# Kernel tuning notes

Hardware: AMD Instinct MI355X
Metric: run time of the kernel (lower is better)

The kernel has to match this reference:

```python
import jax, jax.numpy as jnp
import numpy as np

# Model dims
T, B, J, H, K, N_LAYERS = 512, 64, 256, 256, 25, 3
THETA = 1.0        # spike threshold
SIGMA_INIT = 0.5   # Dcls gaussian sigma (frozen, requires_grad=False)
EPS = 1e-5         # batchnorm eps
ALPHA = 5.0        # ATan surrogate alpha


@jax.custom_vjp
def atan_spike(v):
    # Heaviside forward, ATan surrogate backward (spikingjelly ATan, alpha=5)
    return (v > 0.0).astype(v.dtype)

def _atan_fwd(v):
    return atan_spike(v), v

def _atan_bwd(v, g):
    return (g * (ALPHA / 2.0) / (1.0 + (jnp.pi / 2.0 * ALPHA * v) ** 2),)

atan_spike.defvjp(_atan_fwd, _atan_bwd)


def gauss_kernel(W, P, sig):
    # Dcls1d version='gauss', kernel_count=1: gaussian-interpolated dense kernel.
    # W, P: (O, Jin) -> kernel (O, Jin, K)
    pos = jnp.arange(K, dtype=W.dtype)                  # dilated kernel positions
    c = P + K // 2                                      # shift P into [0, K)
    s = jnp.abs(sig) + 0.27                             # DCLS sigma floor
    g = jnp.exp(-0.5 * ((pos[None, None, :] - c[..., None]) / s) ** 2)
    g = g / (jnp.sum(g, axis=-1, keepdims=True) + 1e-7)  # normalize over positions
    return W[..., None] * g


def delay_lif_layer(x, W, P, beta, gamma, bb, U0):
    # x: (T, B, Jin) -> (T, B, O)
    kern = gauss_kernel(W, P, SIGMA_INIT)               # (O, Jin, K)
    xc = jnp.transpose(x, (1, 2, 0))                    # (B, Jin, T)
    y = jax.lax.conv_general_dilated(
        xc, kern, window_strides=(1,), padding=[(K - 1, 0)],  # causal left-pad
        dimension_numbers=('NCH', 'OIH', 'NCH'))        # (B, O, T)
    y = jnp.transpose(y, (2, 0, 1))                     # (T, B, O)
    # BatchNorm1d over the flattened (T*B) dim, per channel (training stats)
    mu = jnp.mean(y, axis=(0, 1))
    var = jnp.var(y, axis=(0, 1))
    y = (y - mu) * jax.lax.rsqrt(var + EPS) * gamma + bb

    # Soft-reset LIF recurrence over time (note: original passes RAW beta,
    # not sigmoid(beta), to the cell -- reproduced faithfully here).
    def step(carry, xt):
        Ut, St = carry
        Ut = beta * (Ut - THETA * St) + (1.0 - beta) * xt
        St = atan_spike(Ut - THETA)
        return (Ut, St), St

    _, o = jax.lax.scan(step, (U0, jnp.zeros_like(U0)), y)
    return o


def setup_inputs():
    key = jax.random.key(0)
    ks = jax.random.split(key, 5)
    # sparse binary spike input, [T, B, J]
    x = (jax.random.uniform(ks[0], (T, B, J)) < 0.2).astype(jnp.float32)
    bound = float(np.sqrt(6.0 / J))  # kaiming_uniform, relu gain, fan_in = J*1
    W = jax.random.uniform(ks[1], (N_LAYERS, H, J), minval=-bound, maxval=bound, dtype=jnp.float32)
    P = jax.random.uniform(ks[2], (N_LAYERS, H, J), minval=-(K // 2), maxval=K // 2, dtype=jnp.float32)
    beta = jax.random.uniform(ks[3], (N_LAYERS, H), minval=0.7, maxval=0.9, dtype=jnp.float32)
    gamma = jnp.ones((N_LAYERS, H), jnp.float32)
    bb = jnp.zeros((N_LAYERS, H), jnp.float32)
    U0 = jax.random.uniform(ks[4], (N_LAYERS, B, H), dtype=jnp.float32)  # RandomBatchwiseInit(0,1)
    return {"x": x, "W": W, "P": P, "beta": beta, "gamma": gamma, "bb": bb, "U0": U0}


def reference(x, W, P, beta, gamma, bb, U0):
    o = x
    for l in range(N_LAYERS):  # fixed small layer loop
        o = delay_lif_layer(o, W[l], P[l], beta[l], gamma[l], bb[l], U0[l])
    return o
```

## Files before the change

### kernel.cpp

```cpp
#include <hip/hip_runtime.h>
#include <math.h>

#define T_DIM 512
#define B_DIM 64
#define J_DIM 256
#define H_DIM 256
#define K_TAP 25
#define NL    3
#define M_DIM (T_DIM*B_DIM)
#define NBH   (B_DIM*H_DIM)
#define STATB 128
#define GUARD_ROWS 1536
#define GUARD_BYTES (GUARD_ROWS*J_DIM)

#define MB 128
#define NB 64
#define BK 64
#define NST (K_TAP*(J_DIM/BK))
#define BUFB 20480

typedef __attribute__((ext_vector_type(4))) int   i32x4;

__device__ __forceinline__ void gl16(const void* g, void* l){
  __builtin_amdgcn_global_load_lds((const __attribute__((address_space(1))) unsigned int*)g,
                                   (__attribute__((address_space(3))) unsigned int*)l, 16, 0, 0);
}

__global__ void zero_guard_k(unsigned char* __restrict__ g){
  *(uint4*)(g + (size_t)(blockIdx.x*256 + threadIdx.x)*16) = (uint4){0,0,0,0};
}

__global__ void cast_u8_k(const float* __restrict__ x, unsigned char* __restrict__ s){
  const int i = blockIdx.x*256 + threadIdx.x;
  const float4 v = *(const float4*)(x + (size_t)i*4);
  uchar4 o; o.x=(unsigned char)v.x; o.y=(unsigned char)v.y;
  o.z=(unsigned char)v.z; o.w=(unsigned char)v.w;
  *(uchar4*)(s + (size_t)i*4) = o;
}

__global__ void build_kern_k(const float* __restrict__ W, const float* __restrict__ P,
                             signed char* __restrict__ k0, signed char* __restrict__ k1,
                             signed char* __restrict__ k2, float* __restrict__ fsc, int layer){
  __shared__ float red[256];
  const int o = blockIdx.x, j = threadIdx.x;
  const float w = W[(layer*H_DIM + o)*J_DIM + j];
  const float p = P[(layer*H_DIM + o)*J_DIM + j];
  const float c = p + 12.0f;
  const float sg = 0.77f;
  float v[K_TAP]; float ssum = 0.f;
#pragma unroll
  for(int k=0;k<K_TAP;k++){ float z = ((float)k - c)/sg; v[k] = expf(-0.5f*z*z); ssum += v[k]; }
  const float inv = 1.0f/(ssum + 1e-7f);
  float mv = 0.f;
#pragma unroll
  for(int k=0;k<K_TAP;k++){ v[k] = w * (v[k]*inv); mv = fmaxf(mv, fabsf(v[k])); }
  red[j] = mv; __syncthreads();
  for(int st=128; st; st>>=1){ if(j<st) red[j] = fmaxf(red[j], red[j+st]); __syncthreads(); }
  int e; frexpf(red[0], &e);
  const float invq = ldexpf(1.f, 22 - e);
#pragma unroll
  for(int k=0;k<K_TAP;k++){
    const int d = (K_TAP-1)-k;
    int q = (int)lrintf(v[k]*invq);
    const int b0 = (int)(signed char)(q & 0xFF); q = (q - b0) >> 8;
    const int b1 = (int)(signed char)(q & 0xFF); q = (q - b1) >> 8;
    const size_t idx = (size_t)(d*H_DIM + o)*J_DIM + j;
    k0[idx] = (signed char)b0; k1[idx] = (signed char)b1; k2[idx] = (signed char)q;
  }
  if(j==0) fsc[o] = ldexpf(1.f, e - 22);
}

__global__ __launch_bounds__(256,2) void conv_mfma_k(const unsigned char* __restrict__ spk,
    const signed char* __restrict__ k0, const signed char* __restrict__ k1,
    const signed char* __restrict__ k2, const float* __restrict__ fsc,
    float* __restrict__ y){
  __shared__ unsigned char lds[3][BUFB];
  const int tid = threadIdx.x, lane = tid & 63, wave = tid >> 6;
  const int bid = blockIdx.x;
  const int q   = (bid & 7)*128 + (bid >> 3);
  const int m0  = (q & 255) * MB;
  const int n0  = (q >> 8) * NB;
  const int wm0 = (wave >> 1) << 6;
  const int wn0 = (wave & 1) << 5;

  const int srow  = tid >> 2;
  const int sslot = ((tid & 3) ^ (srow >> 1)) & 3;
  const int rslot = ((((lane>>4) ^ (lane>>1)) & 3) << 4);

  i32x4 acc0[4][2], acc1[4][2], acc2[4][2];
#pragma unroll
  for(int m=0;m<4;m++)
#pragma unroll
    for(int n=0;n<2;n++){
      acc0[m][n] = (i32x4){0,0,0,0};
      acc1[m][n] = (i32x4){0,0,0,0};
      acc2[m][n] = (i32x4){0,0,0,0};
    }

#define STAGE(base,t) do{ \
    const int d_ = (t)>>2, jc_ = ((t)&3)<<6; \
    unsigned char* lb_ = (base); \
    const unsigned char* as_ = spk + (size_t)(m0 + srow - (d_<<6) + GUARD_ROWS)*J_DIM + jc_ + sslot*16; \
    gl16(as_,                    lb_        + wave*1024); \
    gl16(as_ + (size_t)64*J_DIM, lb_ + 4096 + wave*1024); \
    const size_t bo_ = (size_t)(d_*H_DIM + n0 + srow)*J_DIM + jc_ + sslot*16; \
    gl16(k0 + bo_, lb_ + 8192  + wave*1024); \
    gl16(k1 + bo_, lb_ + 12288 + wave*1024); \
    gl16(k2 + bo_, lb_ + 16384 + wave*1024); \
  }while(0)

  unsigned char* const L = &lds[0][0];

  STAGE(L, 0);
  STAGE(L + BUFB, 1);

  int rb = 0;
  for(int t=0; t<NST; ++t){
    if(t < NST-1) asm volatile("s_waitcnt vmcnt(5)" ::: "memory");
    else          asm volatile("s_waitcnt vmcnt(0)" ::: "memory");
    __builtin_amdgcn_s_barrier();
    __builtin_amdgcn_sched_barrier(0);
    unsigned char* Lb = L + rb*BUFB;
    i32x4 af[4], b0f[2], b1f[2], b2f[2];
#pragma unroll
    for(int m=0;m<4;m++)
      af[m] = *(const i32x4*)(Lb + (wm0 + m*16 + (lane&15))*64 + rslot);
#pragma unroll
    for(int n=0;n<2;n++){
      const int ro = (wn0 + n*16 + (lane&15))*64 + rslot;
      b0f[n] = *(const i32x4*)(Lb + 8192  + ro);
      b1f[n] = *(const i32x4*)(Lb + 12288 + ro);
      b2f[n] = *(const i32x4*)(Lb + 16384 + ro);
    }
    if(t+2 < NST){
      int sb = rb + 2; if(sb >= 3) sb -= 3;
      STAGE(L + sb*BUFB, t+2);
    }
    __builtin_amdgcn_s_setprio(1);
#pragma unroll
    for(int m=0;m<4;m++)
#pragma unroll
      for(int n=0;n<2;n++){
        acc0[m][n] = __builtin_amdgcn_mfma_i32_16x16x64_i8(af[m], b0f[n], acc0[m][n], 0,0,0);
        acc1[m][n] = __builtin_amdgcn_mfma_i32_16x16x64_i8(af[m], b1f[n], acc1[m][n], 0,0,0);
        acc2[m][n] = __builtin_amdgcn_mfma_i32_16x16x64_i8(af[m], b2f[n], acc2[m][n], 0,0,0);
      }
    __builtin_amdgcn_s_setprio(0);
    rb += 1; if(rb == 3) rb = 0;
  }

  const int r0 = m0 + wm0 + ((lane>>4)<<2);
  const int c0 = n0 + wn0 + (lane&15);
  const double f0 = (double)fsc[c0];
  const double f1 = (double)fsc[c0+16];
#pragma unroll
  for(int m=0;m<4;m++)
#pragma unroll
    for(int n=0;n<2;n++){
      const double fs = n ? f1 : f0;
#pragma unroll
      for(int r=0;r<4;r++){
        const long long cmb = ((long long)acc2[m][n][r] << 16)
                            + ((long long)acc1[m][n][r] << 8)
                            +  (long long)acc0[m][n][r];
        y[(size_t)(r0 + m*16 + r)*H_DIM + c0 + n*16] = (float)((double)cmb * fs);
      }
    }
#undef STAGE
}

__global__ void bn_stats_k(const float* __restrict__ y, double* __restrict__ part){
  const int o   = threadIdx.x;
  const int blk = blockIdx.x;
  const int rows = M_DIM / STATB;
  const float* p = y + (size_t)(blk*rows)*H_DIM + o;
  double s = 0.0, s2 = 0.0;
  for(int r=0;r<rows;r++){
    double v = (double)p[(size_t)r*H_DIM];
    s  += v;
    s2 += v*v;
  }
  part[blk*H_DIM + o]               = s;
  part[STATB*H_DIM + blk*H_DIM + o] = s2;
}

__global__ void bn_final_k(const double* __restrict__ part, float* __restrict__ sc,
                           float* __restrict__ sh, const float* __restrict__ gamma_,
                           const float* __restrict__ bb_, int layer){
  const int o = threadIdx.x;
  double s = 0.0, s2 = 0.0;
  for(int b=0;b<STATB;b++){
    s  += part[b*H_DIM + o];
    s2 += part[STATB*H_DIM + b*H_DIM + o];
  }
  const double inv_n = 1.0 / (double)M_DIM;
  const double m   = s * inv_n;
  const double var = s2 * inv_n - m*m;
  const double rs  = 1.0 / sqrt(var + (double)1e-5f);
  const float g  = gamma_[layer*H_DIM + o];
  const float bv = bb_[layer*H_DIM + o];
  const float scale = (float)((double)g * rs);
  sc[o] = scale;
  sh[o] = (float)((double)bv - m*(double)scale);
}

template<typename TOUT>
__global__ void lif_k(const float* yin, TOUT* sout,
                      const float* __restrict__ sc_, const float* __restrict__ sh_,
                      const float* __restrict__ beta_, const float* __restrict__ U0_,
                      int layer){
  const int idx = blockIdx.x*64 + threadIdx.x;
  const int h = idx & (H_DIM-1);
  const float scale = sc_[h];
  const float shift = sh_[h];
  const float beta  = beta_[layer*H_DIM + h];
  const float ombeta = 1.0f - beta;
  float U = U0_[layer*NBH + idx];
  float S = 0.f;
  float cur[16];
#pragma unroll
  for(int i=0;i<16;i++) cur[i] = yin[(size_t)i*NBH + idx];
  for(int t=0;t<T_DIM;t+=16){
    float nx[16];
#pragma unroll
    for(int i=0;i<16;i++){
      const int tt = t + 16 + i;
      nx[i] = (tt < T_DIM) ? yin[(size_t)tt*NBH + idx] : 0.f;
    }
#pragma unroll
    for(int i=0;i<16;i++){
      const float yv = fmaf(cur[i], scale, shift);
      U = beta*(U - S) + ombeta*yv;
      S = (U > 1.0f) ? 1.f : 0.f;
      sout[(size_t)(t+i)*NBH + idx] = (TOUT)S;
    }
#pragma unroll
    for(int i=0;i<16;i++) cur[i] = nx[i];
  }
}

extern "C" void kernel_launch(void* const* d_in, const int* in_sizes, int n_in,
                              void* d_out, int out_size, void* d_ws, size_t ws_size,
                              hipStream_t stream){
  const float* x    = (const float*)d_in[0];
  const float* W    = (const float*)d_in[1];
  const float* P    = (const float*)d_in[2];
  const float* beta = (const float*)d_in[3];
  const float* gam  = (const float*)d_in[4];
  const float* bb   = (const float*)d_in[5];
  const float* U0   = (const float*)d_in[6];
  float* out = (float*)d_out;

  char* ws = (char*)d_ws;
  unsigned char* spk  = (unsigned char*)ws;
  unsigned char* spkd = spk + GUARD_BYTES;
  signed char*   k0   = (signed char*)(ws + 8781824);
  signed char*   k1   = (signed char*)(ws + 10420224);
  signed char*   k2   = (signed char*)(ws + 12058624);
  float*         fsc  = (float*)(ws + 13697024);
  double*        part = (double*)(ws + 13698048);
  float*         sc   = (float*)(ws + 14222336);
  float*         sh   = sc + 256;

  zero_guard_k<<<dim3(GUARD_BYTES/4096), dim3(256), 0, stream>>>(spk);
  cast_u8_k<<<dim3((M_DIM*J_DIM)/1024), dim3(256), 0, stream>>>(x, spkd);

  for(int l=0;l<NL;l++){
    build_kern_k<<<dim3(H_DIM), dim3(J_DIM), 0, stream>>>(W, P, k0, k1, k2, fsc, l);
    conv_mfma_k<<<dim3((M_DIM/MB)*(H_DIM/NB)), dim3(256), 0, stream>>>(spk, k0, k1, k2, fsc, out);
    bn_stats_k<<<dim3(STATB), dim3(H_DIM), 0, stream>>>(out, part);
    bn_final_k<<<dim3(1), dim3(H_DIM), 0, stream>>>(part, sc, sh, gam, bb, l);
    if(l < NL-1) lif_k<unsigned char><<<dim3(NBH/64), dim3(64), 0, stream>>>(out, spkd, sc, sh, beta, U0, l);
    else         lif_k<float>        <<<dim3(NBH/64), dim3(64), 0, stream>>>(out, out, sc, sh, beta, U0, l);
  }
}
```

Baseline: 579.3 us.

## Load A fragments directly to registers and fuse BN stats into conv epilogue

The conv kernel stops staging the spike (A) tiles through LDS. Each wave now loads its A fragments straight from global memory into double-buffered registers, which shrinks the LDS footprint so three blocks fit per CU. Batchnorm statistics are accumulated in the conv epilogue as exact integer sums, reduced with shuffles and global 64-bit atomics, which removes the separate bn_stats pass over y. The trade-offs are uncoalesced direct global A loads, added register pressure, and atomic contention, with bn_final now resetting the accumulators.

After: 848.1 us. 46.4% more time.

```diff
diff --git a/kernel.cpp b/kernel.cpp
--- a/kernel.cpp
+++ b/kernel.cpp
@@ -9,15 +9,13 @@
 #define NL    3
 #define M_DIM (T_DIM*B_DIM)
 #define NBH   (B_DIM*H_DIM)
-#define STATB 128
 #define GUARD_ROWS 1536
 #define GUARD_BYTES (GUARD_ROWS*J_DIM)
 
 #define MB 128
 #define NB 64
-#define BK 64
-#define NST (K_TAP*(J_DIM/BK))
-#define BUFB 20480
+#define NST (K_TAP*(J_DIM/64))
+#define BSET 12288
 
 typedef __attribute__((ext_vector_type(4))) int   i32x4;
 
@@ -26,8 +24,10 @@
                                    (__attribute__((address_space(3))) unsigned int*)l, 16, 0, 0);
 }
 
-__global__ void zero_guard_k(unsigned char* __restrict__ g){
-  *(uint4*)(g + (size_t)(blockIdx.x*256 + threadIdx.x)*16) = (uint4){0,0,0,0};
+__global__ void zero_guard_k(unsigned char* __restrict__ g, unsigned char* __restrict__ p){
+  const int bid = blockIdx.x;
+  if(bid < 96) *(uint4*)(g + (size_t)(bid*256 + threadIdx.x)*16) = (uint4){0,0,0,0};
+  else         *(uint4*)(p + (size_t)((bid-96)*256 + threadIdx.x)*16) = (uint4){0,0,0,0};
 }
 
 __global__ void cast_u8_k(const float* __restrict__ x, unsigned char* __restrict__ s){
@@ -70,11 +70,11 @@
   if(j==0) fsc[o] = ldexpf(1.f, e - 22);
 }
 
-__global__ __launch_bounds__(256,2) void conv_mfma_k(const unsigned char* __restrict__ spk,
+__global__ __launch_bounds__(256,3) void conv_mfma_k(const unsigned char* __restrict__ spk,
     const signed char* __restrict__ k0, const signed char* __restrict__ k1,
     const signed char* __restrict__ k2, const float* __restrict__ fsc,
-    float* __restrict__ y){
-  __shared__ unsigned char lds[3][BUFB];
+    float* __restrict__ y, long long* __restrict__ part){
+  __shared__ unsigned char lds[3][BSET];
   const int tid = threadIdx.x, lane = tid & 63, wave = tid >> 6;
   const int bid = blockIdx.x;
   const int q   = (bid & 7)*128 + (bid >> 3);
@@ -87,6 +87,9 @@
   const int sslot = ((tid & 3) ^ (srow >> 1)) & 3;
   const int rslot = ((((lane>>4) ^ (lane>>1)) & 3) << 4);
 
+  const unsigned char* abase = spk + (size_t)(m0 + wm0 + (lane&15) + GUARD_ROWS)*J_DIM
+                               + ((lane>>4)<<4);
+
   i32x4 acc0[4][2], acc1[4][2], acc2[4][2];
 #pragma unroll
   for(int m=0;m<4;m++)
@@ -97,56 +100,64 @@
       acc2[m][n] = (i32x4){0,0,0,0};
     }
 
-#define STAGE(base,t) do{ \
+  i32x4 afA[4], afB[4];
+
+#define STAGE_B(base,t) do{ \
     const int d_ = (t)>>2, jc_ = ((t)&3)<<6; \
     unsigned char* lb_ = (base); \
-    const unsigned char* as_ = spk + (size_t)(m0 + srow - (d_<<6) + GUARD_ROWS)*J_DIM + jc_ + sslot*16; \
-    gl16(as_,                    lb_        + wave*1024); \
-    gl16(as_ + (size_t)64*J_DIM, lb_ + 4096 + wave*1024); \
     const size_t bo_ = (size_t)(d_*H_DIM + n0 + srow)*J_DIM + jc_ + sslot*16; \
-    gl16(k0 + bo_, lb_ + 8192  + wave*1024); \
-    gl16(k1 + bo_, lb_ + 12288 + wave*1024); \
-    gl16(k2 + bo_, lb_ + 16384 + wave*1024); \
+    gl16(k0 + bo_, lb_        + wave*1024); \
+    gl16(k1 + bo_, lb_ + 4096 + wave*1024); \
+    gl16(k2 + bo_, lb_ + 8192 + wave*1024); \
   }while(0)
 
-  unsigned char* const L = &lds[0][0];
-
-  STAGE(L, 0);
-  STAGE(L + BUFB, 1);
+#define LOAD_A(AF,t) do{ \
+    const int d_ = (t)>>2, jc_ = ((t)&3)<<6; \
+    const unsigned char* a0_ = abase - (size_t)(d_<<6)*J_DIM + jc_; \
+    AF[0] = *(const i32x4*)(a0_); \
+    AF[1] = *(const i32x4*)(a0_ + 16*J_DIM); \
+    AF[2] = *(const i32x4*)(a0_ + 32*J_DIM); \
+    AF[3] = *(const i32x4*)(a0_ + 48*J_DIM); \
+  }while(0)
+
+#define SUBSTEP(t, AF) do{ \
+    if((t) < NST-1) asm volatile("s_waitcnt vmcnt(3)" ::: "memory"); \
+    else            asm volatile("s_waitcnt vmcnt(0)" ::: "memory"); \
+    __builtin_amdgcn_s_barrier(); \
+    __builtin_amdgcn_sched_barrier(0); \
+    unsigned char* Lb = &lds[0][0] + rb*BSET; \
+    if((t)+2 < NST){ int sb_ = rb + 2; if(sb_ >= 3) sb_ -= 3; STAGE_B(&lds[0][0] + sb_*BSET, (t)+2); } \
+    i32x4 b0f[2], b1f[2], b2f[2]; \
+    _Pragma("unroll") \
+    for(int n=0;n<2;n++){ \
+      const int ro = (wn0 + n*16 + (lane&15))*64 + rslot; \
+      b0f[n] = *(const i32x4*)(Lb + ro); \
+      b1f[n] = *(const i32x4*)(Lb + 4096 + ro); \
+      b2f[n] = *(const i32x4*)(Lb + 8192 + ro); \
+    } \
+    __builtin_amdgcn_s_setprio(1); \
+    _Pragma("unroll") \
+    for(int m=0;m<4;m++) \
+    _Pragma("unroll") \
+      for(int n=0;n<2;n++){ \
+        acc0[m][n] = __builtin_amdgcn_mfma_i32_16x16x64_i8(AF[m], b0f[n], acc0[m][n], 0,0,0); \
+        acc1[m][n] = __builtin_amdgcn_mfma_i32_16x16x64_i8(AF[m], b1f[n], acc1[m][n], 0,0,0); \
+        acc2[m][n] = __builtin_amdgcn_mfma_i32_16x16x64_i8(AF[m], b2f[n], acc2[m][n], 0,0,0); \
+      } \
+    __builtin_amdgcn_s_setprio(0); \
+    if((t)+2 < NST) LOAD_A(AF, (t)+2); \
+    rb += 1; if(rb == 3) rb = 0; \
+  }while(0)
+
+  STAGE_B(&lds[0][0], 0);
+  LOAD_A(afA, 0);
+  STAGE_B(&lds[0][0] + BSET, 1);
+  LOAD_A(afB, 1);
 
   int rb = 0;
-  for(int t=0; t<NST; ++t){
-    if(t < NST-1) asm volatile("s_waitcnt vmcnt(5)" ::: "memory");
-    else          asm volatile("s_waitcnt vmcnt(0)" ::: "memory");
-    __builtin_amdgcn_s_barrier();
-    __builtin_amdgcn_sched_barrier(0);
-    unsigned char* Lb = L + rb*BUFB;
-    i32x4 af[4], b0f[2], b1f[2], b2f[2];
-#pragma unroll
-    for(int m=0;m<4;m++)
-      af[m] = *(const i32x4*)(Lb + (wm0 + m*16 + (lane&15))*64 + rslot);
-#pragma unroll
-    for(int n=0;n<2;n++){
-      const int ro = (wn0 + n*16 + (lane&15))*64 + rslot;
-      b0f[n] = *(const i32x4*)(Lb + 8192  + ro);
-      b1f[n] = *(const i32x4*)(Lb + 12288 + ro);
-      b2f[n] = *(const i32x4*)(Lb + 16384 + ro);
-    }
-    if(t+2 < NST){
-      int sb = rb + 2; if(sb >= 3) sb -= 3;
-      STAGE(L + sb*BUFB, t+2);
-    }
-    __builtin_amdgcn_s_setprio(1);
-#pragma unroll
-    for(int m=0;m<4;m++)
-#pragma unroll
-      for(int n=0;n<2;n++){
-        acc0[m][n] = __builtin_amdgcn_mfma_i32_16x16x64_i8(af[m], b0f[n], acc0[m][n], 0,0,0);
-        acc1[m][n] = __builtin_amdgcn_mfma_i32_16x16x64_i8(af[m], b1f[n], acc1[m][n], 0,0,0);
-        acc2[m][n] = __builtin_amdgcn_mfma_i32_16x16x64_i8(af[m], b2f[n], acc2[m][n], 0,0,0);
-      }
-    __builtin_amdgcn_s_setprio(0);
-    rb += 1; if(rb == 3) rb = 0;
+  for(int t=0; t<NST; t+=2){
+    SUBSTEP(t,   afA);
+    SUBSTEP(t+1, afB);
   }
 
   const int r0 = m0 + wm0 + ((lane>>4)<<2);
@@ -154,48 +165,52 @@
   const double f0 = (double)fsc[c0];
   const double f1 = (double)fsc[c0+16];
 #pragma unroll
-  for(int m=0;m<4;m++)
-#pragma unroll
-    for(int n=0;n<2;n++){
-      const double fs = n ? f1 : f0;
+  for(int n=0;n<2;n++){
+    const double fs = n ? f1 : f0;
+    long long s1 = 0; unsigned long long shi = 0, slo = 0;
+#pragma unroll
+    for(int m=0;m<4;m++)
 #pragma unroll
       for(int r=0;r<4;r++){
         const long long cmb = ((long long)acc2[m][n][r] << 16)
                             + ((long long)acc1[m][n][r] << 8)
                             +  (long long)acc0[m][n][r];
         y[(size_t)(r0 + m*16 + r)*H_DIM + c0 + n*16] = (float)((double)cmb * fs);
+        s1 += cmb;
+        const __int128 sq = (__int128)cmb * cmb;
+        slo += (unsigned long long)(unsigned int)sq;
+        shi += (unsigned long long)(sq >> 32);
       }
-    }
-#undef STAGE
-}
-
-__global__ void bn_stats_k(const float* __restrict__ y, double* __restrict__ part){
-  const int o   = threadIdx.x;
-  const int blk = blockIdx.x;
-  const int rows = M_DIM / STATB;
-  const float* p = y + (size_t)(blk*rows)*H_DIM + o;
-  double s = 0.0, s2 = 0.0;
-  for(int r=0;r<rows;r++){
-    double v = (double)p[(size_t)r*H_DIM];
-    s  += v;
-    s2 += v*v;
-  }
-  part[blk*H_DIM + o]               = s;
-  part[STATB*H_DIM + blk*H_DIM + o] = s2;
-}
-
-__global__ void bn_final_k(const double* __restrict__ part, float* __restrict__ sc,
-                           float* __restrict__ sh, const float* __restrict__ gamma_,
-                           const float* __restrict__ bb_, int layer){
+    s1  += __shfl_xor(s1, 16);  s1  += __shfl_xor(s1, 32);
+    shi += __shfl_xor(shi, 16); shi += __shfl_xor(shi, 32);
+    slo += __shfl_xor(slo, 16); slo += __shfl_xor(slo, 32);
+    if(lane < 16){
+      const int c = c0 + n*16;
+      atomicAdd((unsigned long long*)&part[c],       (unsigned long long)s1);
+      atomicAdd((unsigned long long*)&part[256 + c], shi);
+      atomicAdd((unsigned long long*)&part[512 + c], slo);
+    }
+  }
+#undef STAGE_B
+#undef LOAD_A
+#undef SUBSTEP
+}
+
+__global__ void bn_final_k(long long* __restrict__ part, const float* __restrict__ fsc,
+                           float* __restrict__ sc, float* __restrict__ sh,
+                           const float* __restrict__ gamma_, const float* __restrict__ bb_,
+                           int layer){
   const int o = threadIdx.x;
-  double s = 0.0, s2 = 0.0;
-  for(int b=0;b<STATB;b++){
-    s  += part[b*H_DIM + o];
-    s2 += part[STATB*H_DIM + b*H_DIM + o];
-  }
+  const long long s1           = part[o];
+  const unsigned long long shi = (unsigned long long)part[256 + o];
+  const unsigned long long slo = (unsigned long long)part[512 + o];
+  part[o] = 0; part[256 + o] = 0; part[512 + o] = 0;
+  const double fs  = (double)fsc[o];
+  const double sy  = (double)s1 * fs;
+  const double sy2 = ((double)shi * 4294967296.0 + (double)slo) * fs * fs;
   const double inv_n = 1.0 / (double)M_DIM;
-  const double m   = s * inv_n;
-  const double var = s2 * inv_n - m*m;
+  const double m   = sy * inv_n;
+  const double var = sy2 * inv_n - m*m;
   const double rs  = 1.0 / sqrt(var + (double)1e-5f);
   const float g  = gamma_[layer*H_DIM + o];
   const float bv = bb_[layer*H_DIM + o];
@@ -258,18 +273,17 @@
   signed char*   k1   = (signed char*)(ws + 10420224);
   signed char*   k2   = (signed char*)(ws + 12058624);
   float*         fsc  = (float*)(ws + 13697024);
-  double*        part = (double*)(ws + 13698048);
-  float*         sc   = (float*)(ws + 14222336);
+  long long*     part = (long long*)(ws + 13698048);
+  float*         sc   = (float*)(ws + 13706240);
   float*         sh   = sc + 256;
 
-  zero_guard_k<<<dim3(GUARD_BYTES/4096), dim3(256), 0, stream>>>(spk);
+  zero_guard_k<<<dim3(98), dim3(256), 0, stream>>>(spk, (unsigned char*)part);
   cast_u8_k<<<dim3((M_DIM*J_DIM)/1024), dim3(256), 0, stream>>>(x, spkd);
 
   for(int l=0;l<NL;l++){
     build_kern_k<<<dim3(H_DIM), dim3(J_DIM), 0, stream>>>(W, P, k0, k1, k2, fsc, l);
-    conv_mfma_k<<<dim3((M_DIM/MB)*(H_DIM/NB)), dim3(256), 0, stream>>>(spk, k0, k1, k2, fsc, out);
-    bn_stats_k<<<dim3(STATB), dim3(H_DIM), 0, stream>>>(out, part);
-    bn_final_k<<<dim3(1), dim3(H_DIM), 0, stream>>>(part, sc, sh, gam, bb, l);
+    conv_mfma_k<<<dim3((M_DIM/MB)*(H_DIM/NB)), dim3(256), 0, stream>>>(spk, k0, k1, k2, fsc, out, part);
+    bn_final_k<<<dim3(1), dim3(H_DIM), 0, stream>>>(part, fsc, sc, sh, gam, bb, l);
     if(l < NL-1) lif_k<unsigned char><<<dim3(NBH/64), dim3(64), 0, stream>>>(out, spkd, sc, sh, beta, U0, l);
     else         lif_k<float>        <<<dim3(NBH/64), dim3(64), 0, stream>>>(out, out, sc, sh, beta, U0, l);
   }
```

## Fuse batchnorm statistics into conv epilogue with exact integer atomics

Applied to the files above, without the earlier changes.

Drops the separate bn_stats kernel, which reread the whole 32 MB output per layer. The conv epilogue now accumulates per-channel sums and sums of squares of the exact integer accumulators, reduces them across lanes with shuffles and adds them with 64-bit atomics. bn_final applies the scale factor, splits the squared sum into hi/lo parts and resets the accumulators for the next layer. This adds atomic traffic and epilogue work to the conv kernel, and the guard-zeroing kernel now also clears the atomic buffer.

Measured after the change: 544.0 us. 6.1% less time.

```diff
diff --git a/kernel.cpp b/kernel.cpp
--- a/kernel.cpp
+++ b/kernel.cpp
@@ -9,15 +9,13 @@
 #define NL    3
 #define M_DIM (T_DIM*B_DIM)
 #define NBH   (B_DIM*H_DIM)
-#define STATB 128
 #define GUARD_ROWS 1536
 #define GUARD_BYTES (GUARD_ROWS*J_DIM)
 
 #define MB 128
 #define NB 64
-#define BK 64
-#define NST (K_TAP*(J_DIM/BK))
-#define BUFB 20480
+#define NST (K_TAP*(J_DIM/64))
+#define BSET 20480
 
 typedef __attribute__((ext_vector_type(4))) int   i32x4;
 
@@ -26,8 +24,10 @@
                                    (__attribute__((address_space(3))) unsigned int*)l, 16, 0, 0);
 }
 
-__global__ void zero_guard_k(unsigned char* __restrict__ g){
-  *(uint4*)(g + (size_t)(blockIdx.x*256 + threadIdx.x)*16) = (uint4){0,0,0,0};
+__global__ void zero_guard_k(unsigned char* __restrict__ g, unsigned char* __restrict__ p){
+  const int bid = blockIdx.x;
+  if(bid < 96) *(uint4*)(g + (size_t)(bid*256 + threadIdx.x)*16) = (uint4){0,0,0,0};
+  else         *(uint4*)(p + (size_t)((bid-96)*256 + threadIdx.x)*16) = (uint4){0,0,0,0};
 }
 
 __global__ void cast_u8_k(const float* __restrict__ x, unsigned char* __restrict__ s){
@@ -73,8 +73,8 @@
 __global__ __launch_bounds__(256,2) void conv_mfma_k(const unsigned char* __restrict__ spk,
     const signed char* __restrict__ k0, const signed char* __restrict__ k1,
     const signed char* __restrict__ k2, const float* __restrict__ fsc,
-    float* __restrict__ y){
-  __shared__ unsigned char lds[3][BUFB];
+    float* __restrict__ y, long long* __restrict__ part){
+  __shared__ unsigned char lds[3][BSET];
   const int tid = threadIdx.x, lane = tid & 63, wave = tid >> 6;
   const int bid = blockIdx.x;
   const int q   = (bid & 7)*128 + (bid >> 3);
@@ -112,7 +112,7 @@
   unsigned char* const L = &lds[0][0];
 
   STAGE(L, 0);
-  STAGE(L + BUFB, 1);
+  STAGE(L + BSET, 1);
 
   int rb = 0;
   for(int t=0; t<NST; ++t){
@@ -120,7 +120,7 @@
     else          asm volatile("s_waitcnt vmcnt(0)" ::: "memory");
     __builtin_amdgcn_s_barrier();
     __builtin_amdgcn_sched_barrier(0);
-    unsigned char* Lb = L + rb*BUFB;
+    unsigned char* Lb = L + rb*BSET;
     i32x4 af[4], b0f[2], b1f[2], b2f[2];
 #pragma unroll
     for(int m=0;m<4;m++)
@@ -134,7 +134,7 @@
     }
     if(t+2 < NST){
       int sb = rb + 2; if(sb >= 3) sb -= 3;
-      STAGE(L + sb*BUFB, t+2);
+      STAGE(L + sb*BSET, t+2);
     }
     __builtin_amdgcn_s_setprio(1);
 #pragma unroll
@@ -154,48 +154,50 @@
   const double f0 = (double)fsc[c0];
   const double f1 = (double)fsc[c0+16];
 #pragma unroll
-  for(int m=0;m<4;m++)
-#pragma unroll
-    for(int n=0;n<2;n++){
-      const double fs = n ? f1 : f0;
+  for(int n=0;n<2;n++){
+    const double fs = n ? f1 : f0;
+    long long s1 = 0; unsigned long long shi = 0, slo = 0;
+#pragma unroll
+    for(int m=0;m<4;m++)
 #pragma unroll
       for(int r=0;r<4;r++){
         const long long cmb = ((long long)acc2[m][n][r] << 16)
                             + ((long long)acc1[m][n][r] << 8)
                             +  (long long)acc0[m][n][r];
         y[(size_t)(r0 + m*16 + r)*H_DIM + c0 + n*16] = (float)((double)cmb * fs);
+        s1 += cmb;
+        const __int128 sq = (__int128)cmb * cmb;
+        slo += (unsigned long long)(unsigned int)sq;
+        shi += (unsigned long long)(sq >> 32);
       }
-    }
+    s1  += __shfl_xor(s1, 16);  s1  += __shfl_xor(s1, 32);
+    shi += __shfl_xor(shi, 16); shi += __shfl_xor(shi, 32);
+    slo += __shfl_xor(slo, 16); slo += __shfl_xor(slo, 32);
+    if(lane < 16){
+      const int c = c0 + n*16;
+      atomicAdd((unsigned long long*)&part[c],       (unsigned long long)s1);
+      atomicAdd((unsigned long long*)&part[256 + c], shi);
+      atomicAdd((unsigned long long*)&part[512 + c], slo);
+    }
+  }
 #undef STAGE
 }
 
-__global__ void bn_stats_k(const float* __restrict__ y, double* __restrict__ part){
-  const int o   = threadIdx.x;
-  const int blk = blockIdx.x;
-  const int rows = M_DIM / STATB;
-  const float* p = y + (size_t)(blk*rows)*H_DIM + o;
-  double s = 0.0, s2 = 0.0;
-  for(int r=0;r<rows;r++){
-    double v = (double)p[(size_t)r*H_DIM];
-    s  += v;
-    s2 += v*v;
-  }
-  part[blk*H_DIM + o]               = s;
-  part[STATB*H_DIM + blk*H_DIM + o] = s2;
-}
-
-__global__ void bn_final_k(const double* __restrict__ part, float* __restrict__ sc,
-                           float* __restrict__ sh, const float* __restrict__ gamma_,
-                           const float* __restrict__ bb_, int layer){
+__global__ void bn_final_k(long long* __restrict__ part, const float* __restrict__ fsc,
+                           float* __restrict__ sc, float* __restrict__ sh,
+                           const float* __restrict__ gamma_, const float* __restrict__ bb_,
+                           int layer){
   const int o = threadIdx.x;
-  double s = 0.0, s2 = 0.0;
-  for(int b=0;b<STATB;b++){
-    s  += part[b*H_DIM + o];
-    s2 += part[STATB*H_DIM + b*H_DIM + o];
-  }
+  const long long s1           = part[o];
+  const unsigned long long shi = (unsigned long long)part[256 + o];
+  const unsigned long long slo = (unsigned long long)part[512 + o];
+  part[o] = 0; part[256 + o] = 0; part[512 + o] = 0;
+  const double fs  = (double)fsc[o];
+  const double sy  = (double)s1 * fs;
+  const double sy2 = ((double)shi * 4294967296.0 + (double)slo) * fs * fs;
   const double inv_n = 1.0 / (double)M_DIM;
-  const double m   = s * inv_n;
-  const double var = s2 * inv_n - m*m;
+  const double m   = sy * inv_n;
+  const double var = sy2 * inv_n - m*m;
   const double rs  = 1.0 / sqrt(var + (double)1e-5f);
   const float g  = gamma_[layer*H_DIM + o];
   const float bv = bb_[layer*H_DIM + o];
@@ -258,18 +260,17 @@
   signed char*   k1   = (signed char*)(ws + 10420224);
   signed char*   k2   = (signed char*)(ws + 12058624);
   float*         fsc  = (float*)(ws + 13697024);
-  double*        part = (double*)(ws + 13698048);
-  float*         sc   = (float*)(ws + 14222336);
+  long long*     part = (long long*)(ws + 13698048);
+  float*         sc   = (float*)(ws + 13706240);
   float*         sh   = sc + 256;
 
-  zero_guard_k<<<dim3(GUARD_BYTES/4096), dim3(256), 0, stream>>>(spk);
+  zero_guard_k<<<dim3(98), dim3(256), 0, stream>>>(spk, (unsigned char*)part);
   cast_u8_k<<<dim3((M_DIM*J_DIM)/1024), dim3(256), 0, stream>>>(x, spkd);
 
   for(int l=0;l<NL;l++){
     build_kern_k<<<dim3(H_DIM), dim3(J_DIM), 0, stream>>>(W, P, k0, k1, k2, fsc, l);
-    conv_mfma_k<<<dim3((M_DIM/MB)*(H_DIM/NB)), dim3(256), 0, stream>>>(spk, k0, k1, k2, fsc, out);
-    bn_stats_k<<<dim3(STATB), dim3(H_DIM), 0, stream>>>(out, part);
-    bn_final_k<<<dim3(1), dim3(H_DIM), 0, stream>>>(part, sc, sh, gam, bb, l);
+    conv_mfma_k<<<dim3((M_DIM/MB)*(H_DIM/NB)), dim3(256), 0, stream>>>(spk, k0, k1, k2, fsc, out, part);
+    bn_final_k<<<dim3(1), dim3(H_DIM), 0, stream>>>(part, fsc, sc, sh, gam, bb, l);
     if(l < NL-1) lif_k<unsigned char><<<dim3(NBH/64), dim3(64), 0, stream>>>(out, spkd, sc, sh, beta, U0, l);
     else         lif_k<float>        <<<dim3(NBH/64), dim3(64), 0, stream>>>(out, out, sc, sh, beta, U0, l);
   }
```
